# Kernel optimization log

Measured on AMD Instinct MI355X. Metric: run time of the kernel, lower is better.

Reference implementation:

```python
import jax, jax.numpy as jnp
import numpy as np

N = 100000
C = 32            # channels per degree (shape_in == shape_out == 32)
NI = C * C        # flattened Gram-matrix size = n_input = n_hidden
LN_EPS = 1e-5
SLOPE = 0.01      # LeakyReLU default negative slope


def _ln(x, g, b):
    mu = jnp.mean(x, axis=-1, keepdims=True)
    var = jnp.var(x, axis=-1, keepdims=True)  # biased, matches torch LayerNorm
    return (x - mu) * jax.lax.rsqrt(var + LN_EPS) * g + b


def _lrelu(x):
    return jnp.where(x >= 0, x, SLOPE * x)


def _gal(v, g1, b1, w1, g2, b2, w2, bias2):
    # v: [N, ch_in, m]
    n, ci, _ = v.shape
    dot = jnp.einsum('nac,nbc->nab', v, v).reshape(n, ci * ci)  # Gram matrix
    dot = jnp.sign(dot) * jnp.maximum(jnp.abs(dot), 1e-12)
    h = _lrelu(_ln(dot, g1, b1)) @ w1.T           # [N, ch_in*ch_out]
    h = _lrelu(_ln(h, g2, b2)) @ w2.T + bias2      # [N, ch_in*ch_out]
    attn = jax.nn.softmax(h.reshape(n, -1, ci), axis=-1)  # [N, ch_out, ch_in]
    return jnp.einsum('nab,nbc->nac', attn, v)     # [N, ch_out, m]


def _mk_type_params(key):
    ks = jax.random.split(key, 3)
    bound = np.sqrt(6.0 / NI)  # kaiming_uniform_, fan_in=NI
    return dict(
        ln1_g=jnp.ones((NI,), jnp.float32),
        ln1_b=jnp.zeros((NI,), jnp.float32),
        w1=jax.random.uniform(ks[0], (NI, NI), jnp.float32, -bound, bound),
        ln2_g=jnp.ones((NI,), jnp.float32),
        ln2_b=jnp.zeros((NI,), jnp.float32),
        w2=jax.random.uniform(ks[1], (NI, NI), jnp.float32, -bound, bound),
        b2=jax.random.uniform(ks[2], (NI,), jnp.float32, -1.0 / C, 1.0 / C),
    )


def setup_inputs():
    key = jax.random.key(0)
    k0, k1, kp0, kp1 = jax.random.split(key, 4)
    d = {
        'f0': jax.random.normal(k0, (N, C, 1), jnp.float32),
        'f1': jax.random.normal(k1, (N, C, 3), jnp.float32),
    }
    for tag, kk in (('0', kp0), ('1', kp1)):
        p = _mk_type_params(kk)
        for name, val in p.items():
            d[f'{name}_{tag}'] = val
    return d


def reference(f0, f1,
              ln1_g_0, ln1_b_0, w1_0, ln2_g_0, ln2_b_0, w2_0, b2_0,
              ln1_g_1, ln1_b_1, w1_1, ln2_g_1, ln2_b_1, w2_1, b2_1):
    out0 = _gal(f0, ln1_g_0, ln1_b_0, w1_0, ln2_g_0, ln2_b_0, w2_0, b2_0)
    out1 = _gal(f1, ln1_g_1, ln1_b_1, w1_1, ln2_g_1, ln2_b_1, w2_1, b2_1)
    return (out0, out1)
```

## Files before the change

kernel.cpp:

```cpp
#include <hip/hip_runtime.h>

#define NN     100000
#define NB     1563
#define LN_EPS 1e-5f
#define SLOPE  0.01f

typedef __bf16 bf16x8 __attribute__((ext_vector_type(8)));
typedef float  f32x4  __attribute__((ext_vector_type(4)));
typedef unsigned short u16;
typedef unsigned int   u32;

union Pack8 { uint4 u4; bf16x8 bf; u16 s[8]; };

__device__ __forceinline__ u16 f2bf(float x){
    u32 b = __float_as_uint(x);
    b += 0x7fffu + ((b >> 16) & 1u);
    return (u16)(b >> 16);
}

__global__ __launch_bounds__(1024) void prep_weights(
    const float* __restrict__ wa, const float* __restrict__ wb,
    const float* __restrict__ wc, const float* __restrict__ wd,
    u16* __restrict__ dst)
{
    int m = blockIdx.y;
    const float* src = (m==0)? wa : (m==1)? wb : (m==2)? wc : wd;
    u16* d = dst + (size_t)m * (1024u*1024u);
    int tid = blockIdx.x * blockDim.x + threadIdx.x;
    int sub = tid & 3;
    int row = (tid >> 2) & 1023;
    int kb  = tid >> 12;
    const float4* s4 = (const float4*)(src + row*1024 + kb*32 + sub*8);
    float4 a = s4[0], b = s4[1];
    Pack8 p;
    p.s[0]=f2bf(a.x); p.s[1]=f2bf(a.y); p.s[2]=f2bf(a.z); p.s[3]=f2bf(a.w);
    p.s[4]=f2bf(b.x); p.s[5]=f2bf(b.y); p.s[6]=f2bf(b.z); p.s[7]=f2bf(b.w);
    ((uint4*)d)[(kb*1024 + row)*4 + sub] = p.u4;
}

__device__ __forceinline__ void gemm_quad1(
    const u16* __restrict__ Wp, const u16* xs,
    int C0, int lane15, int q, f32x4 acc[4][4])
{
    const uint4* bb = (const uint4*)Wp + (C0 + lane15)*4 + q;
    const uint4* ab = (const uint4*)xs + q*64 + lane15;
    #pragma unroll
    for (int t=0; t<4; ++t)
      #pragma unroll
      for (int rt=0; rt<4; ++rt)
        acc[t][rt] = (f32x4){0.f,0.f,0.f,0.f};
    #pragma unroll 2
    for (int ks=0; ks<32; ++ks){
        Pack8 b[4], a[4];
        #pragma unroll
        for (int t=0; t<4; ++t) b[t].u4 = bb[ks*4096 + t*64];
        #pragma unroll
        for (int rt=0; rt<4; ++rt) a[rt].u4 = ab[ks*256 + rt*16];
        #pragma unroll
        for (int t=0; t<4; ++t)
          #pragma unroll
          for (int rt=0; rt<4; ++rt)
            acc[t][rt] = __builtin_amdgcn_mfma_f32_16x16x32_bf16(a[rt].bf, b[t].bf, acc[t][rt], 0,0,0);
    }
}

template<int MDIM>
__global__ __launch_bounds__(1024, 4) void gal_fused(
    const float* __restrict__ f,
    const float* __restrict__ ln1g, const float* __restrict__ ln1b,
    const float* __restrict__ ln2g, const float* __restrict__ ln2b,
    const float* __restrict__ b2,
    const u16* __restrict__ Wp1, const u16* __restrict__ Wp2,
    float* __restrict__ outp)
{
    extern __shared__ char smem[];
    constexpr int VSTR = 32*MDIM + 4;
    constexpr int SBS  = 64*32 + 4;
    u16*   xs    = (u16*)smem;
    float* sbuf  = (float*)smem;
    float* vbuf  = (float*)smem + 32832;
    float* stats = (float*)smem + 32832 + 64*VSTR;

    const int tid    = threadIdx.x;
    const int lane   = tid & 63;
    const int wv     = tid >> 6;
    const int lane15 = lane & 15;
    const int q      = lane >> 4;
    const int node0  = blockIdx.x * 64;

    if (tid < 128) stats[tid] = 0.f;
    {
        float4* vbuf4 = (float4*)vbuf;
        const int gv4  = node0*8*MDIM;
        const int lim4 = NN*8*MDIM;
        for (int i = tid; i < 64*8*MDIM; i += 1024){
            int nd = i / (8*MDIM);
            int r4 = i - nd*(8*MDIM);
            float4 val = (gv4 + i < lim4) ? ((const float4*)f)[gv4 + i]
                                          : (float4){0.f,0.f,0.f,0.f};
            vbuf4[nd*(VSTR/4) + r4] = val;
        }
    }
    __syncthreads();

    {
        const int n = tid >> 4;
        const int j = tid & 15;
        const float* vn = vbuf + n*VSTR;
        float va[2][MDIM];
        #pragma unroll
        for (int c=0;c<MDIM;++c){ va[0][c]=vn[(j*2)*MDIM+c]; va[1][c]=vn[(j*2+1)*MDIM+c]; }
        float sum=0.f, ssum=0.f;
        #pragma unroll
        for (int b=0;b<32;++b){
            float d0=0.f, d1=0.f;
            #pragma unroll
            for (int c=0;c<MDIM;++c){ float vb = vn[b*MDIM+c]; d0 += va[0][c]*vb; d1 += va[1][c]*vb; }
            sum += d0+d1; ssum += d0*d0 + d1*d1;
        }
        #pragma unroll
        for (int st=1; st<16; st<<=1){ sum += __shfl_xor(sum, st); ssum += __shfl_xor(ssum, st); }
        float mu   = sum * (1.f/1024.f);
        float rstd = rsqrtf(ssum*(1.f/1024.f) - mu*mu + LN_EPS);
        #pragma unroll
        for (int jb=0;jb<8;++jb){
            Pack8 p;
            const int ai = jb >> 2;
            #pragma unroll
            for (int l=0;l<8;++l){
                int b = (jb*8+l) & 31;
                float d = 0.f;
                #pragma unroll
                for (int c=0;c<MDIM;++c) d += va[ai][c]*vn[b*MDIM+c];
                int k = j*64 + jb*8 + l;
                float x = (d - mu)*rstd*ln1g[k] + ln1b[k];
                x = (x >= 0.f)? x : SLOPE*x;
                p.s[l] = f2bf(x);
            }
            ((uint4*)xs)[(j*8+jb)*64 + n] = p.u4;
        }
    }
    __syncthreads();

    {
        f32x4 acc[4][4];
        gemm_quad1(Wp1, xs, wv*64, lane15, q, acc);
        {
            float p_[16], pp_[16];
            #pragma unroll
            for (int idx=0; idx<16; ++idx){
                int rt = idx>>2, rr = idx&3;
                float s=0.f, s2=0.f;
                #pragma unroll
                for (int t=0; t<4; ++t){ float h = acc[t][rt][rr]; s += h; s2 += h*h; }
                p_[idx] = s; pp_[idx] = s2;
            }
            #pragma unroll
            for (int m=8; m>=1; m>>=1){
                const bool hi = (lane15 & m) != 0;
                #pragma unroll
                for (int i=0; i<m; ++i){
                    float sp = hi ? p_[i]  : p_[i+m];
                    float kp = hi ? p_[i+m]  : p_[i];
                    p_[i]  = kp + __shfl_xor(sp, m);
                    float sq = hi ? pp_[i] : pp_[i+m];
                    float kq = hi ? pp_[i+m] : pp_[i];
                    pp_[i] = kq + __shfl_xor(sq, m);
                }
            }
            int nd = (lane15>>2)*16 + q*4 + (lane15&3);
            atomicAdd(&stats[2*nd],   p_[0]);
            atomicAdd(&stats[2*nd+1], pp_[0]);
        }
        __syncthreads();

        float g2c[4], b2c[4];
        #pragma unroll
        for (int t=0; t<4; ++t){
            int col = wv*64 + t*16 + lane15;
            g2c[t] = ln2g[col];
            b2c[t] = ln2b[col];
        }
        #pragma unroll
        for (int rt=0; rt<4; ++rt)
          #pragma unroll
          for (int rr=0; rr<4; ++rr){
            int nd = rt*16 + q*4 + rr;
            float mu   = stats[2*nd]*(1.f/1024.f);
            float rstd = rsqrtf(stats[2*nd+1]*(1.f/1024.f) - mu*mu + LN_EPS);
            #pragma unroll
            for (int t=0; t<4; ++t){
                float h = acc[t][rt][rr];
                float x = (h - mu)*rstd*g2c[t] + b2c[t];
                x = (x >= 0.f)? x : SLOPE*x;
                int col = wv*64 + t*16 + lane15;
                xs[(col>>3)*512 + nd*8 + (col&7)] = f2bf(x);
            }
          }
    }
    __syncthreads();

    {
        f32x4 acc[4][4];
        gemm_quad1(Wp2, xs, wv*64, lane15, q, acc);
        float bias[4];
        #pragma unroll
        for (int t=0; t<4; ++t)
            bias[t] = b2[wv*64 + t*16 + lane15];
        __syncthreads();

        #pragma unroll
        for (int ps=0; ps<2; ++ps){
            #pragma unroll
            for (int ctl=0; ctl<2; ++ctl){
                const int t = ps*2 + ctl;
                #pragma unroll
                for (int rt=0; rt<4; ++rt)
                  #pragma unroll
                  for (int rr=0; rr<4; ++rr){
                    int nd = rt*16 + q*4 + rr;
                    sbuf[wv*SBS + nd*32 + ctl*16 + lane15] = acc[t][rt][rr] + bias[t];
                  }
            }
            __syncthreads();
            {
                const int nd = tid >> 4;
                const int s  = tid & 15;
                const float* hp = sbuf + s*SBS + nd*32;
                float e[32];
                #pragma unroll
                for (int r=0;r<8;++r){
                    float4 v4 = ((const float4*)hp)[r];
                    e[4*r]=v4.x; e[4*r+1]=v4.y; e[4*r+2]=v4.z; e[4*r+3]=v4.w;
                }
                float mx = e[0];
                #pragma unroll
                for (int b=1;b<32;++b) mx = fmaxf(mx, e[b]);
                float sm = 0.f;
                #pragma unroll
                for (int b=0;b<32;++b){ e[b] = __expf(e[b]-mx); sm += e[b]; }
                float inv = 1.f / sm;
                float oacc[MDIM];
                #pragma unroll
                for (int c=0;c<MDIM;++c) oacc[c]=0.f;
                const float4* vr = (const float4*)(vbuf + nd*VSTR);
                #pragma unroll
                for (int r=0; r<8*MDIM; ++r){
                    float4 v4 = vr[r];
                    #pragma unroll
                    for (int t=0;t<4;++t){
                        const int fi = 4*r+t;
                        const int b  = fi/MDIM;
                        const int c  = fi - b*MDIM;
                        float comp = (t==0)?v4.x:(t==1)?v4.y:(t==2)?v4.z:v4.w;
                        oacc[c] += e[b]*comp;
                    }
                }
                int ng = node0 + nd;
                if (ng < NN){
                    const int a = s*2 + ps;
                    #pragma unroll
                    for (int c=0;c<MDIM;++c)
                        outp[((size_t)ng*32 + a)*MDIM + c] = oacc[c]*inv;
                }
            }
            if (ps==0) __syncthreads();
        }
    }
}

extern "C" void kernel_launch(void* const* d_in, const int* in_sizes, int n_in,
                              void* d_out, int out_size, void* d_ws, size_t ws_size,
                              hipStream_t stream)
{
    const float* f0    = (const float*)d_in[0];
    const float* f1    = (const float*)d_in[1];
    const float* ln1g0 = (const float*)d_in[2];
    const float* ln1b0 = (const float*)d_in[3];
    const float* w1_0  = (const float*)d_in[4];
    const float* ln2g0 = (const float*)d_in[5];
    const float* ln2b0 = (const float*)d_in[6];
    const float* w2_0  = (const float*)d_in[7];
    const float* b2_0  = (const float*)d_in[8];
    const float* ln1g1 = (const float*)d_in[9];
    const float* ln1b1 = (const float*)d_in[10];
    const float* w1_1  = (const float*)d_in[11];
    const float* ln2g1 = (const float*)d_in[12];
    const float* ln2b1 = (const float*)d_in[13];
    const float* w2_1  = (const float*)d_in[14];
    const float* b2_1  = (const float*)d_in[15];
    float* out = (float*)d_out;
    u16* wp = (u16*)d_ws;

    const int smem1 = (32832 + 64*(32*1+4) + 128)*4;
    const int smem3 = (32832 + 64*(32*3+4) + 128)*4;
    (void)hipFuncSetAttribute(reinterpret_cast<const void*>(&gal_fused<1>),
                              hipFuncAttributeMaxDynamicSharedMemorySize, smem1);
    (void)hipFuncSetAttribute(reinterpret_cast<const void*>(&gal_fused<3>),
                              hipFuncAttributeMaxDynamicSharedMemorySize, smem3);

    prep_weights<<<dim3(128,4), 1024, 0, stream>>>(w1_0, w2_0, w1_1, w2_1, wp);
    gal_fused<1><<<NB, 1024, smem1, stream>>>(f0, ln1g0, ln1b0, ln2g0, ln2b0, b2_0,
                                              wp,            wp + 1048576, out);
    gal_fused<3><<<NB, 1024, smem3, stream>>>(f1, ln1g1, ln1b1, ln2g1, ln2b1, b2_1,
                                              wp + 2097152,  wp + 3145728, out + (size_t)NN*32);
}
```

Baseline: 1.380 ms.

## Merge both degree kernels into one launch and stage coalesced output stores

The two per-degree kernels become one launch that interleaves type-0 and type-1 blocks, which removes the tail and launch gap between them. Every block now reserves the larger type-1 shared-memory size. The Gram computation keeps all 64 dot products in registers and reads V as float4, so it no longer recomputes them for the LayerNorm output. The softmax/attention output is written to shared memory first and then stored to global memory in coalesced order instead of strided scattered writes, at the cost of extra barriers and more register pressure.

```diff
diff --git a/kernel.cpp b/kernel.cpp
--- a/kernel.cpp
+++ b/kernel.cpp
@@ -65,7 +65,8 @@
 }
 
 template<int MDIM>
-__global__ __launch_bounds__(1024, 4) void gal_fused(
+__device__ __forceinline__ void gal_body(
+    const int blk, char* smem,
     const float* __restrict__ f,
     const float* __restrict__ ln1g, const float* __restrict__ ln1b,
     const float* __restrict__ ln2g, const float* __restrict__ ln2b,
@@ -73,7 +74,6 @@
     const u16* __restrict__ Wp1, const u16* __restrict__ Wp2,
     float* __restrict__ outp)
 {
-    extern __shared__ char smem[];
     constexpr int VSTR = 32*MDIM + 4;
     constexpr int SBS  = 64*32 + 4;
     u16*   xs    = (u16*)smem;
@@ -86,7 +86,7 @@
     const int wv     = tid >> 6;
     const int lane15 = lane & 15;
     const int q      = lane >> 4;
-    const int node0  = blockIdx.x * 64;
+    const int node0  = blk * 64;
 
     if (tid < 128) stats[tid] = 0.f;
     {
@@ -109,14 +109,30 @@
         const float* vn = vbuf + n*VSTR;
         float va[2][MDIM];
         #pragma unroll
-        for (int c=0;c<MDIM;++c){ va[0][c]=vn[(j*2)*MDIM+c]; va[1][c]=vn[(j*2+1)*MDIM+c]; }
+        for (int c=0;c<MDIM;++c){ va[0][c]=vn[(2*j)*MDIM+c]; va[1][c]=vn[(2*j+1)*MDIM+c]; }
+        float d0[32], d1[32];
+        #pragma unroll
+        for (int b=0;b<32;++b){ d0[b]=0.f; d1[b]=0.f; }
+        constexpr int NF4 = (32*MDIM)/4;
+        const float4* vn4 = (const float4*)vn;
+        #pragma unroll
+        for (int fq=0; fq<NF4; ++fq){
+            float4 q4 = vn4[fq];
+            #pragma unroll
+            for (int e=0;e<4;++e){
+                const int fi = 4*fq + e;
+                const int b  = fi / MDIM;
+                const int c  = fi % MDIM;
+                const float vbc = (e==0)?q4.x:(e==1)?q4.y:(e==2)?q4.z:q4.w;
+                d0[b] += va[0][c]*vbc;
+                d1[b] += va[1][c]*vbc;
+            }
+        }
         float sum=0.f, ssum=0.f;
         #pragma unroll
         for (int b=0;b<32;++b){
-            float d0=0.f, d1=0.f;
-            #pragma unroll
-            for (int c=0;c<MDIM;++c){ float vb = vn[b*MDIM+c]; d0 += va[0][c]*vb; d1 += va[1][c]*vb; }
-            sum += d0+d1; ssum += d0*d0 + d1*d1;
+            sum  += d0[b] + d1[b];
+            ssum += d0[b]*d0[b] + d1[b]*d1[b];
         }
         #pragma unroll
         for (int st=1; st<16; st<<=1){ sum += __shfl_xor(sum, st); ssum += __shfl_xor(ssum, st); }
@@ -125,13 +141,10 @@
         #pragma unroll
         for (int jb=0;jb<8;++jb){
             Pack8 p;
-            const int ai = jb >> 2;
             #pragma unroll
             for (int l=0;l<8;++l){
-                int b = (jb*8+l) & 31;
-                float d = 0.f;
-                #pragma unroll
-                for (int c=0;c<MDIM;++c) d += va[ai][c]*vn[b*MDIM+c];
+                const int bb = (jb*8+l) & 31;
+                float d = (jb>>2) ? d1[bb] : d0[bb];
                 int k = j*64 + jb*8 + l;
                 float x = (d - mu)*rstd*ln1g[k] + ln1b[k];
                 x = (x >= 0.f)? x : SLOPE*x;
@@ -210,28 +223,30 @@
         __syncthreads();
 
         #pragma unroll
-        for (int ps=0; ps<2; ++ps){
-            #pragma unroll
-            for (int ctl=0; ctl<2; ++ctl){
-                const int t = ps*2 + ctl;
-                #pragma unroll
-                for (int rt=0; rt<4; ++rt)
-                  #pragma unroll
-                  for (int rr=0; rr<4; ++rr){
-                    int nd = rt*16 + q*4 + rr;
-                    sbuf[wv*SBS + nd*32 + ctl*16 + lane15] = acc[t][rt][rr] + bias[t];
-                  }
+        for (int r=0; r<2; ++r){
+            if ((wv>>3) == r){
+                #pragma unroll
+                for (int t=0; t<4; ++t){
+                    const int slot = (wv&7)*2 + (t>>1);
+                    #pragma unroll
+                    for (int rt=0; rt<4; ++rt)
+                      #pragma unroll
+                      for (int rr=0; rr<4; ++rr){
+                        int nd = rt*16 + q*4 + rr;
+                        sbuf[slot*SBS + nd*32 + (t&1)*16 + lane15] = acc[t][rt][rr] + bias[t];
+                      }
+                }
             }
             __syncthreads();
             {
                 const int nd = tid >> 4;
                 const int s  = tid & 15;
-                const float* hp = sbuf + s*SBS + nd*32;
+                float* hp = sbuf + s*SBS + nd*32;
                 float e[32];
                 #pragma unroll
-                for (int r=0;r<8;++r){
-                    float4 v4 = ((const float4*)hp)[r];
-                    e[4*r]=v4.x; e[4*r+1]=v4.y; e[4*r+2]=v4.z; e[4*r+3]=v4.w;
+                for (int rr=0;rr<8;++rr){
+                    float4 v4 = ((const float4*)hp)[rr];
+                    e[4*rr]=v4.x; e[4*rr+1]=v4.y; e[4*rr+2]=v4.z; e[4*rr+3]=v4.w;
                 }
                 float mx = e[0];
                 #pragma unroll
@@ -245,28 +260,59 @@
                 for (int c=0;c<MDIM;++c) oacc[c]=0.f;
                 const float4* vr = (const float4*)(vbuf + nd*VSTR);
                 #pragma unroll
-                for (int r=0; r<8*MDIM; ++r){
-                    float4 v4 = vr[r];
+                for (int rr=0; rr<8*MDIM; ++rr){
+                    float4 v4 = vr[rr];
                     #pragma unroll
                     for (int t=0;t<4;++t){
-                        const int fi = 4*r+t;
+                        const int fi = 4*rr+t;
                         const int b  = fi/MDIM;
                         const int c  = fi - b*MDIM;
                         float comp = (t==0)?v4.x:(t==1)?v4.y:(t==2)?v4.z:v4.w;
                         oacc[c] += e[b]*comp;
                     }
                 }
-                int ng = node0 + nd;
-                if (ng < NN){
-                    const int a = s*2 + ps;
-                    #pragma unroll
-                    for (int c=0;c<MDIM;++c)
-                        outp[((size_t)ng*32 + a)*MDIM + c] = oacc[c]*inv;
-                }
-            }
-            if (ps==0) __syncthreads();
-        }
-    }
+                #pragma unroll
+                for (int c=0;c<MDIM;++c) hp[c] = oacc[c]*inv;
+            }
+            __syncthreads();
+            {
+                const int CH = 64*16*MDIM;
+                for (int i = tid; i < CH; i += 1024){
+                    int nd, rem;
+                    if (MDIM==1){ nd = i >> 4; rem = i & 15; }
+                    else        { nd = i / (16*MDIM); rem = i - nd*(16*MDIM); }
+                    const int s = rem / MDIM;
+                    const int c = rem - s*MDIM;
+                    const int ng = node0 + nd;
+                    if (ng < NN)
+                        outp[(size_t)ng*(32*MDIM) + r*(16*MDIM) + rem]
+                            = sbuf[s*SBS + nd*32 + c];
+                }
+            }
+            if (r==0) __syncthreads();
+        }
+    }
+}
+
+__global__ __launch_bounds__(1024, 4) void gal_fused_all(
+    const float* __restrict__ f0, const float* __restrict__ f1,
+    const float* __restrict__ ln1g0, const float* __restrict__ ln1b0,
+    const float* __restrict__ ln2g0, const float* __restrict__ ln2b0,
+    const float* __restrict__ b2_0,
+    const float* __restrict__ ln1g1, const float* __restrict__ ln1b1,
+    const float* __restrict__ ln2g1, const float* __restrict__ ln2b1,
+    const float* __restrict__ b2_1,
+    const u16* __restrict__ wp, float* __restrict__ out)
+{
+    extern __shared__ char smem[];
+    const int gid = blockIdx.x;
+    const int blk = gid >> 1;
+    if ((gid & 1) == 0)
+        gal_body<1>(blk, smem, f0, ln1g0, ln1b0, ln2g0, ln2b0, b2_0,
+                    wp,            wp + 1048576, out);
+    else
+        gal_body<3>(blk, smem, f1, ln1g1, ln1b1, ln2g1, ln2b1, b2_1,
+                    wp + 2097152,  wp + 3145728, out + (size_t)NN*32);
 }
 
 extern "C" void kernel_launch(void* const* d_in, const int* in_sizes, int n_in,
@@ -292,16 +338,13 @@
     float* out = (float*)d_out;
     u16* wp = (u16*)d_ws;
 
-    const int smem1 = (32832 + 64*(32*1+4) + 128)*4;
-    const int smem3 = (32832 + 64*(32*3+4) + 128)*4;
-    (void)hipFuncSetAttribute(reinterpret_cast<const void*>(&gal_fused<1>),
-                              hipFuncAttributeMaxDynamicSharedMemorySize, smem1);
-    (void)hipFuncSetAttribute(reinterpret_cast<const void*>(&gal_fused<3>),
-                              hipFuncAttributeMaxDynamicSharedMemorySize, smem3);
+    const int smem = (32832 + 64*(32*3+4) + 128)*4;
+    (void)hipFuncSetAttribute(reinterpret_cast<const void*>(&gal_fused_all),
+                              hipFuncAttributeMaxDynamicSharedMemorySize, smem);
 
     prep_weights<<<dim3(128,4), 1024, 0, stream>>>(w1_0, w2_0, w1_1, w2_1, wp);
-    gal_fused<1><<<NB, 1024, smem1, stream>>>(f0, ln1g0, ln1b0, ln2g0, ln2b0, b2_0,
-                                              wp,            wp + 1048576, out);
-    gal_fused<3><<<NB, 1024, smem3, stream>>>(f1, ln1g1, ln1b1, ln2g1, ln2b1, b2_1,
-                                              wp + 2097152,  wp + 3145728, out + (size_t)NN*32);
-}
+    gal_fused_all<<<2*NB, 1024, smem, stream>>>(f0, f1,
+        ln1g0, ln1b0, ln2g0, ln2b0, b2_0,
+        ln1g1, ln1b1, ln2g1, ln2b1, b2_1,
+        wp, out);
+}
```

Result: slower. 1.449 ms (+5.0%).

## Merge both degree kernels into one launch and stage output through LDS

Applied to the files above, without the earlier changes.

Combines the two per-degree fused kernels into a single grid of 2*NB blocks, where the first half handles degree-1 and the second half degree-0. This removes one kernel launch and the tail bubble between the two launches. The softmax-weighted outputs are now kept in registers, written to shared memory as a contiguous per-node image, and stored to global memory with coalesced float4 writes instead of strided scalar stores. In exchange, every block reserves the larger degree-1 shared memory size, which may lower occupancy for the degree-0 blocks, and the extra staging pass adds a barrier.

```diff
diff --git a/kernel.cpp b/kernel.cpp
--- a/kernel.cpp
+++ b/kernel.cpp
@@ -65,7 +65,8 @@
 }
 
 template<int MDIM>
-__global__ __launch_bounds__(1024, 4) void gal_fused(
+__device__ __forceinline__ void gal_body(
+    const int blk, char* smem,
     const float* __restrict__ f,
     const float* __restrict__ ln1g, const float* __restrict__ ln1b,
     const float* __restrict__ ln2g, const float* __restrict__ ln2b,
@@ -73,7 +74,6 @@
     const u16* __restrict__ Wp1, const u16* __restrict__ Wp2,
     float* __restrict__ outp)
 {
-    extern __shared__ char smem[];
     constexpr int VSTR = 32*MDIM + 4;
     constexpr int SBS  = 64*32 + 4;
     u16*   xs    = (u16*)smem;
@@ -86,7 +86,7 @@
     const int wv     = tid >> 6;
     const int lane15 = lane & 15;
     const int q      = lane >> 4;
-    const int node0  = blockIdx.x * 64;
+    const int node0  = blk * 64;
 
     if (tid < 128) stats[tid] = 0.f;
     {
@@ -209,6 +209,10 @@
             bias[t] = b2[wv*64 + t*16 + lane15];
         __syncthreads();
 
+        const int nd_c = tid >> 4;
+        const int s_c  = tid & 15;
+        float keep[2][MDIM];
+
         #pragma unroll
         for (int ps=0; ps<2; ++ps){
             #pragma unroll
@@ -224,9 +228,7 @@
             }
             __syncthreads();
             {
-                const int nd = tid >> 4;
-                const int s  = tid & 15;
-                const float* hp = sbuf + s*SBS + nd*32;
+                const float* hp = sbuf + s_c*SBS + nd_c*32;
                 float e[32];
                 #pragma unroll
                 for (int r=0;r<8;++r){
@@ -243,7 +245,7 @@
                 float oacc[MDIM];
                 #pragma unroll
                 for (int c=0;c<MDIM;++c) oacc[c]=0.f;
-                const float4* vr = (const float4*)(vbuf + nd*VSTR);
+                const float4* vr = (const float4*)(vbuf + nd_c*VSTR);
                 #pragma unroll
                 for (int r=0; r<8*MDIM; ++r){
                     float4 v4 = vr[r];
@@ -256,17 +258,52 @@
                         oacc[c] += e[b]*comp;
                     }
                 }
-                int ng = node0 + nd;
-                if (ng < NN){
-                    const int a = s*2 + ps;
-                    #pragma unroll
-                    for (int c=0;c<MDIM;++c)
-                        outp[((size_t)ng*32 + a)*MDIM + c] = oacc[c]*inv;
-                }
-            }
-            if (ps==0) __syncthreads();
-        }
-    }
+                #pragma unroll
+                for (int c=0;c<MDIM;++c) keep[ps][c] = oacc[c]*inv;
+            }
+            __syncthreads();
+        }
+
+        {
+            float* img = sbuf;
+            #pragma unroll
+            for (int c=0;c<MDIM;++c){
+                img[nd_c*(32*MDIM) + (2*s_c  )*MDIM + c] = keep[0][c];
+                img[nd_c*(32*MDIM) + (2*s_c+1)*MDIM + c] = keep[1][c];
+            }
+        }
+        __syncthreads();
+
+        {
+            const float4* img4 = (const float4*)sbuf;
+            float4* out4 = (float4*)(outp + (size_t)node0*(32*MDIM));
+            constexpr int NPV = 8*MDIM;
+            for (int i = tid; i < 64*NPV; i += 1024){
+                int nd = (MDIM==1) ? (i >> 3) : (i / NPV);
+                if (node0 + nd < NN) out4[i] = img4[i];
+            }
+        }
+    }
+}
+
+__global__ __launch_bounds__(1024, 4) void gal_fused_all(
+    const float* __restrict__ f0, const float* __restrict__ f1,
+    const float* __restrict__ ln1g0, const float* __restrict__ ln1b0,
+    const float* __restrict__ ln2g0, const float* __restrict__ ln2b0,
+    const float* __restrict__ b2_0,
+    const float* __restrict__ ln1g1, const float* __restrict__ ln1b1,
+    const float* __restrict__ ln2g1, const float* __restrict__ ln2b1,
+    const float* __restrict__ b2_1,
+    const u16* __restrict__ wp, float* __restrict__ out)
+{
+    extern __shared__ char smem[];
+    const int gid = blockIdx.x;
+    if (gid < NB)
+        gal_body<3>(gid, smem, f1, ln1g1, ln1b1, ln2g1, ln2b1, b2_1,
+                    wp + 2097152,  wp + 3145728, out + (size_t)NN*32);
+    else
+        gal_body<1>(gid - NB, smem, f0, ln1g0, ln1b0, ln2g0, ln2b0, b2_0,
+                    wp,            wp + 1048576, out);
 }
 
 extern "C" void kernel_launch(void* const* d_in, const int* in_sizes, int n_in,
@@ -292,16 +329,13 @@
     float* out = (float*)d_out;
     u16* wp = (u16*)d_ws;
 
-    const int smem1 = (32832 + 64*(32*1+4) + 128)*4;
-    const int smem3 = (32832 + 64*(32*3+4) + 128)*4;
-    (void)hipFuncSetAttribute(reinterpret_cast<const void*>(&gal_fused<1>),
-                              hipFuncAttributeMaxDynamicSharedMemorySize, smem1);
-    (void)hipFuncSetAttribute(reinterpret_cast<const void*>(&gal_fused<3>),
-                              hipFuncAttributeMaxDynamicSharedMemorySize, smem3);
+    const int smem = (32832 + 64*(32*3+4) + 128)*4;
+    (void)hipFuncSetAttribute(reinterpret_cast<const void*>(&gal_fused_all),
+                              hipFuncAttributeMaxDynamicSharedMemorySize, smem);
 
     prep_weights<<<dim3(128,4), 1024, 0, stream>>>(w1_0, w2_0, w1_1, w2_1, wp);
-    gal_fused<1><<<NB, 1024, smem1, stream>>>(f0, ln1g0, ln1b0, ln2g0, ln2b0, b2_0,
-                                              wp,            wp + 1048576, out);
-    gal_fused<3><<<NB, 1024, smem3, stream>>>(f1, ln1g1, ln1b1, ln2g1, ln2b1, b2_1,
-                                              wp + 2097152,  wp + 3145728, out + (size_t)NN*32);
-}
+    gal_fused_all<<<2*NB, 1024, smem, stream>>>(f0, f1,
+        ln1g0, ln1b0, ln2g0, ln2b0, b2_0,
+        ln1g1, ln1b1, ln2g1, ln2b1, b2_1,
+        wp, out);
+}
```

Measured after the change: 1.331 ms. 3.5% less time.
